# Kernel optimization log

Measured on AMD Instinct MI355X. Metric: run time of the kernel, lower is better.

Reference implementation:

```python
import jax, jax.numpy as jnp
import numpy as np

B, S, HID = 2, 2048, 2048
NH, NKV, D = 32, 8, 128
EPS = 1e-06
ROPE_BASE = 1000000.0


def _rope_tables(seq_len, dim, base):
    inv_freq = 1.0 / (base ** (jnp.arange(0, dim, 2, dtype=jnp.float32) / dim))
    t = jnp.arange(seq_len, dtype=jnp.float32)
    freqs = jnp.einsum('i,j->ij', t, inv_freq)          # [S, D/2]
    emb = jnp.concatenate([freqs, freqs], axis=-1)      # [S, D]
    return emb[None, None].astype(jnp.float32)          # [1,1,S,D] (pre cos/sin)


def setup_inputs() -> dict:
    key = jax.random.key(0)
    ks = jax.random.split(key, 6)
    emb = _rope_tables(S, D, ROPE_BASE)
    return {
        'hidden_states': jax.random.normal(ks[0], (B, S, HID), jnp.float32),
        'cos': jnp.cos(emb),
        'sin': jnp.sin(emb),
        'wq': jax.random.normal(ks[1], (NH * D, HID), jnp.float32) * 0.02,
        'wk': jax.random.normal(ks[2], (NKV * D, HID), jnp.float32) * 0.02,
        'wv': jax.random.normal(ks[3], (NKV * D, HID), jnp.float32) * 0.02,
        'wo': jax.random.normal(ks[4], (HID, NH * D), jnp.float32) * 0.02,
        'q_norm_w': jnp.ones((D,), jnp.float32),
        'k_norm_w': jnp.ones((D,), jnp.float32),
    }


def _rmsnorm(x, w, eps=EPS):
    xf = x.astype(jnp.float32)
    var = jnp.mean(xf * xf, axis=-1, keepdims=True)
    return (w * (xf * jax.lax.rsqrt(var + eps))).astype(x.dtype)


def _rotate_half(x):
    x1, x2 = jnp.split(x, 2, axis=-1)
    return jnp.concatenate([-x2, x1], axis=-1)


def reference(hidden_states, cos, sin, wq, wk, wv, wo, q_norm_w, k_norm_w):
    b, s, _ = hidden_states.shape
    groups = NH // NKV
    # projections -> [b, heads, s, d]
    q = (hidden_states @ wq.T).reshape(b, s, NH, D).transpose(0, 2, 1, 3)
    k = (hidden_states @ wk.T).reshape(b, s, NKV, D).transpose(0, 2, 1, 3)
    v = (hidden_states @ wv.T).reshape(b, s, NKV, D).transpose(0, 2, 1, 3)
    # per-head RMSNorm then RoPE
    q = _rmsnorm(q, q_norm_w)
    k = _rmsnorm(k, k_norm_w)
    q = q * cos + _rotate_half(q) * sin
    k = k * cos + _rotate_half(k) * sin
    # GQA expansion (repeat_interleave on head dim)
    k = jnp.repeat(k, groups, axis=1)
    v = jnp.repeat(v, groups, axis=1)
    # attention scores with additive causal bias of -10000 (as in source)
    scores = jnp.einsum('bhqd,bhkd->bhqk', q, k) / jnp.sqrt(jnp.float32(D))
    mask = jnp.triu(jnp.ones((s, s), jnp.float32), k=1)
    scores = scores - mask * 10000.0
    attn = jax.nn.softmax(scores.astype(jnp.float32), axis=-1).astype(q.dtype)
    out = jnp.einsum('bhqk,bhkd->bhqd', attn, v)
    out = out.transpose(0, 2, 1, 3).reshape(b, s, NH * D)
    return out @ wo.T
```

## Files before the change

### kernel.cpp

```cpp
#include <hip/hip_runtime.h>

typedef unsigned short u16;
typedef __attribute__((ext_vector_type(8))) short bf16x8;
typedef __attribute__((ext_vector_type(4))) float f32x4;
typedef __attribute__((ext_vector_type(2))) unsigned int u32x2;
typedef __attribute__((ext_vector_type(4))) unsigned int u32x4;

#define GAS __attribute__((address_space(1)))
#define LAS __attribute__((address_space(3)))
#define MFMA __builtin_amdgcn_mfma_f32_16x16x32_bf16
#define BAR() __builtin_amdgcn_s_barrier()
#define WAITV(n) asm volatile("s_waitcnt vmcnt(" #n ")" ::: "memory")

__device__ __forceinline__ void gload16(const void* g, void* l) {
  __builtin_amdgcn_global_load_lds((GAS void*)g, (LAS void*)l, 16, 0, 0);
}
__device__ __forceinline__ u16 f2b(float x) {
  union { float f; unsigned u; } c; c.f = x;
  unsigned r = c.u + 0x7fffu + ((c.u >> 16) & 1u);
  return (u16)(r >> 16);
}
__device__ __forceinline__ float b2f(u16 h) {
  union { unsigned u; float f; } c; c.u = ((unsigned)h) << 16;
  return c.f;
}
__device__ __forceinline__ unsigned cvtpk(float lo, float hi) {
  unsigned r;
  asm("v_cvt_pk_bf16_f32 %0, %1, %2" : "=v"(r) : "v"(lo), "v"(hi));
  return r;
}

__global__ __launch_bounds__(256) void cvt_all(
    const float* __restrict__ hs, const float* __restrict__ wq,
    const float* __restrict__ wk, const float* __restrict__ wv,
    const float* __restrict__ wo, u16* __restrict__ hsb,
    u16* __restrict__ wqkv, u16* __restrict__ wob) {
  int i = blockIdx.x * 256 + threadIdx.x;
  const float* src;
  u16* dst;
  int off;
  if (i < 1048576) {
    src = hs; dst = hsb; off = i;
  } else if (i < 2097152) {
    src = wq; dst = wqkv; off = i - 1048576;
  } else if (i < 2359296) {
    src = wk; dst = wqkv + 8388608; off = i - 2097152;
  } else if (i < 2621440) {
    src = wv; dst = wqkv + 10485760; off = i - 2359296;
  } else {
    src = wo; dst = wob; off = i - 2621440;
  }
  const float4* s4 = (const float4*)src;
  float4 a = s4[(size_t)off * 2], b = s4[(size_t)off * 2 + 1];
  u32x4 v;
  v[0] = (unsigned)f2b(a.x) | ((unsigned)f2b(a.y) << 16);
  v[1] = (unsigned)f2b(a.z) | ((unsigned)f2b(a.w) << 16);
  v[2] = (unsigned)f2b(b.x) | ((unsigned)f2b(b.y) << 16);
  v[3] = (unsigned)f2b(b.z) | ((unsigned)f2b(b.w) << 16);
  *(u32x4*)(dst + (size_t)off * 8) = v;
}

template <int MODE>
__global__ __launch_bounds__(512, 2) void gemm256(
    const u16* __restrict__ A, const u16* __restrict__ B,
    u16* __restrict__ Dq, u16* __restrict__ Dk, u16* __restrict__ Dv,
    float* __restrict__ Dout, float* __restrict__ Daux,
    const float* __restrict__ cosT, const float* __restrict__ sinT,
    const float* __restrict__ qnw, const float* __restrict__ knw,
    int Kstride, int KLEN, int tilesN, int nwg) {
  __shared__ __attribute__((aligned(16))) u16 lds[2][2][2][128 * 64];
  __shared__ float ssl[4][256];
  const int tid = threadIdx.x;
  const int lane = tid & 63;
  const int w = tid >> 6;
  const int wr = w >> 2, wc = w & 3;
  const int r = lane & 15, g = lane >> 4;

  int wg = blockIdx.x;
  const int cpx = nwg >> 3;
  wg = (wg & 7) * cpx + (wg >> 3);
  int sk = 0;
  if (MODE == 1) { sk = wg >> 7; wg &= 127; }
  const int bx = wg % tilesN, by = wg / tilesN;
  const size_t m0 = (size_t)by * 256, n0 = (size_t)bx * 256;
  const size_t koff = (size_t)sk * KLEN;
  const int NT = KLEN >> 6;

  auto stage = [&](int dbuf, int op, int half, int c, int k0) {
    int slot = c * 512 + tid;
    int row = slot >> 3;
    int kg = (slot & 7) ^ (row & 7);
    const u16* src = (op == 0)
        ? A + (m0 + half * 128 + row) * (size_t)Kstride + koff + k0 + kg * 8
        : B + (n0 + half * 128 + row) * (size_t)Kstride + koff + k0 + kg * 8;
    gload16(src, (char*)&lds[dbuf][op][half][0] + c * 8192 + w * 1024);
  };
  auto ldA = [&](int cur, int mi, int kk) -> bf16x8 {
    int rowl = mi * 16 + r;
    return *(const bf16x8*)((const char*)&lds[cur][0][wr][0] + rowl * 128 +
                            (((kk << 2) + g) ^ (rowl & 7)) * 16);
  };
  auto ldB = [&](int cur, int ni, int kk) -> bf16x8 {
    int rowl = (wc & 1) * 64 + ni * 16 + r;
    return *(const bf16x8*)((const char*)&lds[cur][1][wc >> 1][0] + rowl * 128 +
                            (((kk << 2) + g) ^ (rowl & 7)) * 16);
  };

  f32x4 acc[8][4];
#pragma unroll
  for (int i = 0; i < 8; ++i)
#pragma unroll
    for (int j = 0; j < 4; ++j) acc[i][j] = (f32x4){0.f, 0.f, 0.f, 0.f};

  stage(0, 1, 0, 0, 0); stage(0, 1, 0, 1, 0);
  stage(0, 1, 1, 0, 0); stage(0, 1, 1, 1, 0);
  stage(0, 0, 0, 0, 0); stage(0, 0, 1, 0, 0);
  stage(0, 0, 0, 1, 0); stage(0, 0, 1, 1, 0);
  WAITV(2);
  BAR();

  bf16x8 bf_[4][2];

#define GPHASE(MI0, IS0, IS1, WAITCODE)                                    \
  {                                                                        \
    bf16x8 aA0 = ldA(cur, MI0, 0), aA1 = ldA(cur, MI0, 1);                 \
    bf16x8 aB0 = ldA(cur, MI0 + 1, 0), aB1 = ldA(cur, MI0 + 1, 1);         \
    IS0; IS1;                                                              \
    BAR();                                                                 \
    __builtin_amdgcn_s_setprio(1);                                         \
    _Pragma("unroll") for (int ni = 0; ni < 4; ++ni) {                     \
      acc[MI0][ni] = MFMA(aA0, bf_[ni][0], acc[MI0][ni], 0, 0, 0);         \
      acc[MI0][ni] = MFMA(aA1, bf_[ni][1], acc[MI0][ni], 0, 0, 0);         \
      acc[MI0 + 1][ni] = MFMA(aB0, bf_[ni][0], acc[MI0 + 1][ni], 0, 0, 0); \
      acc[MI0 + 1][ni] = MFMA(aB1, bf_[ni][1], acc[MI0 + 1][ni], 0, 0, 0); \
    }                                                                      \
    __builtin_amdgcn_s_setprio(0);                                         \
    WAITCODE;                                                              \
    BAR();                                                                 \
  }

  for (int t = 0; t < NT - 1; ++t) {
    const int cur = t & 1, nb = cur ^ 1;
    const int k1 = (t + 1) << 6;
#pragma unroll
    for (int ni = 0; ni < 4; ++ni) {
      bf_[ni][0] = ldB(cur, ni, 0);
      bf_[ni][1] = ldB(cur, ni, 1);
    }
    GPHASE(0, stage(nb, 1, 0, 0, k1), stage(nb, 1, 0, 1, k1), );
    GPHASE(2, stage(nb, 1, 1, 0, k1), stage(nb, 1, 1, 1, k1), WAITV(4));
    GPHASE(4, stage(nb, 0, 0, 0, k1), stage(nb, 0, 1, 0, k1), );
    GPHASE(6, stage(nb, 0, 0, 1, k1), stage(nb, 0, 1, 1, k1), WAITV(2));
  }
  {
    const int cur = (NT - 1) & 1;
#pragma unroll
    for (int ni = 0; ni < 4; ++ni) {
      bf_[ni][0] = ldB(cur, ni, 0);
      bf_[ni][1] = ldB(cur, ni, 1);
    }
    GPHASE(0, , , );
    GPHASE(2, , , WAITV(0));
    GPHASE(4, , , );
    GPHASE(6, , , );
  }
#undef GPHASE

  if (MODE == 1) {
    float* pbase = (sk == 0) ? Dout : Daux;
#pragma unroll
    for (int mi = 0; mi < 8; ++mi)
#pragma unroll
      for (int ni = 0; ni < 4; ++ni)
#pragma unroll
        for (int j = 0; j < 4; ++j) {
          int m = (int)m0 + wr * 128 + mi * 16 + g * 4 + j;
          int n = (int)n0 + wc * 64 + ni * 16 + r;
          pbase[(size_t)m * (size_t)(tilesN * 256) + n] = acc[mi][ni][j];
        }
    return;
  }

  u16* lt = (u16*)&lds[0][0][0][0];

  if (bx < 20) {
    const bool isQ = (bx < 16);
    const float* nw = isQ ? qnw : knw;
    const float osc = isQ ? (0.08838834764831845f * 1.4426950408889634f) : 1.0f;

#pragma unroll
    for (int mi = 0; mi < 8; ++mi)
#pragma unroll
      for (int j = 0; j < 4; ++j) {
        float sq = 0.f;
#pragma unroll
        for (int ni = 0; ni < 4; ++ni) {
          float v = acc[mi][ni][j];
          sq += v * v;
        }
        sq += __shfl_xor(sq, 1);
        sq += __shfl_xor(sq, 2);
        sq += __shfl_xor(sq, 4);
        sq += __shfl_xor(sq, 8);
        ssl[wc][wr * 128 + mi * 16 + g * 4 + j] = sq;
      }
    BAR();

#pragma unroll
    for (int mi = 0; mi < 8; ++mi)
#pragma unroll
      for (int j = 0; j < 4; ++j) {
        int ml = wr * 128 + mi * 16 + g * 4 + j;
        float ss = ssl[wc & 2][ml] + ssl[(wc & 2) | 1][ml];
        float inv = rsqrtf(ss * (1.0f / 128.0f) + 1e-6f);
#pragma unroll
        for (int ni = 0; ni < 4; ++ni) {
          int d = (wc & 1) * 64 + ni * 16 + r;
          lt[ml * 256 + wc * 64 + ni * 16 + r] = f2b(acc[mi][ni][j] * inv * nw[d]);
        }
      }
    BAR();

#pragma unroll
    for (int t8 = 0; t8 < 8; ++t8) {
      int task = t8 * 512 + tid;
      int ml = task >> 4;
      int hd = (task >> 3) & 1;
      int gp = task & 7;
      int d0 = gp * 8;
      u32x4 xl = *(const u32x4*)(lt + ml * 256 + hd * 128 + d0);
      u32x4 xh = *(const u32x4*)(lt + ml * 256 + hd * 128 + 64 + d0);
      int m = (int)m0 + ml;
      int b = m >> 11, s = m & 2047;
      const float* cb = cosT + s * 128 + d0;
      const float* sb = sinT + s * 128 + d0;
      float4 c0a = *(const float4*)(cb), c0b = *(const float4*)(cb + 4);
      float4 s0a = *(const float4*)(sb), s0b = *(const float4*)(sb + 4);
      float4 c1a = *(const float4*)(cb + 64), c1b = *(const float4*)(cb + 68);
      float4 s1a = *(const float4*)(sb + 64), s1b = *(const float4*)(sb + 68);
      float x0[8], x1[8];
#pragma unroll
      for (int e = 0; e < 4; ++e) {
        x0[2 * e] = b2f((u16)(xl[e] & 0xffffu));
        x0[2 * e + 1] = b2f((u16)(xl[e] >> 16));
        x1[2 * e] = b2f((u16)(xh[e] & 0xffffu));
        x1[2 * e + 1] = b2f((u16)(xh[e] >> 16));
      }
      float c0[8] = {c0a.x, c0a.y, c0a.z, c0a.w, c0b.x, c0b.y, c0b.z, c0b.w};
      float s0[8] = {s0a.x, s0a.y, s0a.z, s0a.w, s0b.x, s0b.y, s0b.z, s0b.w};
      float c1[8] = {c1a.x, c1a.y, c1a.z, c1a.w, c1b.x, c1b.y, c1b.z, c1b.w};
      float s1[8] = {s1a.x, s1a.y, s1a.z, s1a.w, s1b.x, s1b.y, s1b.z, s1b.w};
      u32x4 y0, y1;
#pragma unroll
      for (int e = 0; e < 4; ++e) {
        float a0 = (x0[2 * e] * c0[2 * e] - x1[2 * e] * s0[2 * e]) * osc;
        float a1 = (x0[2 * e + 1] * c0[2 * e + 1] - x1[2 * e + 1] * s0[2 * e + 1]) * osc;
        y0[e] = cvtpk(a0, a1);
        float b0 = (x1[2 * e] * c1[2 * e] + x0[2 * e] * s1[2 * e]) * osc;
        float b1 = (x1[2 * e + 1] * c1[2 * e + 1] + x0[2 * e + 1] * s1[2 * e + 1]) * osc;
        y1[e] = cvtpk(b0, b1);
      }
      if (isQ) {
        int hq = 2 * bx + hd;
        u16* dst = Dq + (((size_t)b * 32 + hq) * 2048 + s) * 128 + d0;
        *(u32x4*)dst = y0;
        *(u32x4*)(dst + 64) = y1;
      } else {
        int hk = 2 * (bx - 16) + hd;
        u16* dst = Dk + (((size_t)b * 8 + hk) * 2048 + s) * 128 + d0;
        *(u32x4*)dst = y0;
        *(u32x4*)(dst + 64) = y1;
      }
    }
  } else {
#pragma unroll
    for (int mi = 0; mi < 8; ++mi)
#pragma unroll
      for (int ni = 0; ni < 4; ++ni)
#pragma unroll
        for (int j = 0; j < 4; ++j) {
          int ml = wr * 128 + mi * 16 + g * 4 + j;
          int nl = wc * 64 + ni * 16 + r;
          int gm = ml >> 3;
          lt[nl * 256 + (((gm ^ (nl & 7)) << 3) | (ml & 7))] = f2b(acc[mi][ni][j]);
        }
    BAR();
#pragma unroll
    for (int t16 = 0; t16 < 16; ++t16) {
      int task = t16 * 512 + tid;
      int nl = task >> 5;
      int mg = task & 31;
      u32x4 v = *(const u32x4*)(lt + nl * 256 + ((mg ^ (nl & 7)) << 3));
      int hv = 2 * (bx - 20) + (nl >> 7);
      int d = nl & 127;
      int m = (int)m0 + mg * 8;
      int b = m >> 11, s = m & 2047;
      *(u32x4*)(Dv + (((size_t)b * 8 + hv) * 128 + d) * 2048 + s) = v;
    }
  }
}

__global__ __launch_bounds__(256) void reduce_add(const float* __restrict__ P0,
                                                  const float* __restrict__ P1,
                                                  float* __restrict__ out, int n4) {
  int i = blockIdx.x * 256 + threadIdx.x;
  if (i >= n4) return;
  float4 a = ((const float4*)P0)[i];
  float4 b = ((const float4*)P1)[i];
  a.x += b.x; a.y += b.y; a.z += b.z; a.w += b.w;
  ((float4*)out)[i] = a;
}

__global__ __launch_bounds__(256, 2) void attn_fwd(const u16* __restrict__ Q,
                                                   const u16* __restrict__ Kg,
                                                   const u16* __restrict__ Vg,
                                                   u16* __restrict__ AO) {
  __shared__ __attribute__((aligned(16))) u16 Ks[2][64 * 128];
  __shared__ __attribute__((aligned(16))) u16 Vt[2][128 * 64];
  __shared__ __attribute__((aligned(16))) u16 Plds[4][32 * 64];
  const int tid = threadIdx.x;
  const int lane = tid & 63;
  const int w = tid >> 6;
  const int r = lane & 15, g = lane >> 4;
  const int p = blockIdx.x, h = blockIdx.y, b = blockIdx.z;
  const int hkv = h >> 2;

  const u16* Kp = Kg + (((size_t)b * 8 + hkv) * 2048) * 128;
  const u16* Vp = Vg + (((size_t)b * 8 + hkv) * 128) * 2048;

  const short one_bf = (short)0x3F80;
  const bf16x8 vones = {one_bf, one_bf, one_bf, one_bf, one_bf, one_bf, one_bf, one_bf};

#pragma unroll 1
  for (int phase = 0; phase < 2; ++phase) {
    const int qt = phase == 0 ? (15 - p) : p;
    const u16* Qp = Q + (((size_t)b * 32 + h) * 2048 + qt * 128 + w * 32) * 128;

    bf16x8 qf[2][4];
#pragma unroll
    for (int f = 0; f < 2; ++f)
#pragma unroll
      for (int kk = 0; kk < 4; ++kk)
        qf[f][kk] = *(const bf16x8*)(Qp + (f * 16 + r) * 128 + kk * 32 + g * 8);

    f32x4 off[2][8];
#pragma unroll
    for (int f = 0; f < 2; ++f)
#pragma unroll
      for (int i = 0; i < 8; ++i) off[f][i] = (f32x4){0.f, 0.f, 0.f, 0.f};
    f32x4 lr4[2] = {(f32x4){0.f, 0.f, 0.f, 0.f}, (f32x4){0.f, 0.f, 0.f, 0.f}};
    const int qg0 = qt * 128 + w * 32 + r;
    const int qg1 = qg0 + 16;

    const u16* kst[4];
    const u16* vst[4];
#pragma unroll
    for (int c = 0; c < 4; ++c) {
      int t = c * 256 + tid;
      kst[c] = Kp + (size_t)(t >> 4) * 128 + (size_t)(((t & 15) ^ ((t >> 4) & 7)) * 8);
      int d = t >> 3;
      vst[c] = Vp + (size_t)d * 2048 + (size_t)(((t & 7) ^ ((d >> 1) & 7)) * 8);
    }
    auto stageKV = [&](int buf) {
#pragma unroll
      for (int c = 0; c < 4; ++c) {
        gload16(kst[c], (char*)&Ks[buf][0] + c * 4096 + w * 1024);
        kst[c] += 64 * 128;
      }
#pragma unroll
      for (int c = 0; c < 4; ++c) {
        gload16(vst[c], (char*)&Vt[buf][0] + c * 4096 + w * 1024);
        vst[c] += 64;
      }
    };

    const int nu = 2 * qt + 2;

    stageKV(0);
    WAITV(0);
    BAR();

    for (int kt = 0; kt < nu; ++kt) {
      const int cur = kt & 1;
      if (kt + 1 < nu) stageKV(cur ^ 1);

      const char* KsC = (const char*)&Ks[cur][0];
      const char* VtC = (const char*)&Vt[cur][0];

      f32x4 sc0[4], sc1[4];
#pragma unroll
      for (int ni = 0; ni < 4; ++ni) {
        f32x4 a0 = (f32x4){0.f, 0.f, 0.f, 0.f};
        f32x4 a1 = (f32x4){0.f, 0.f, 0.f, 0.f};
        int ro = ni * 16 + r;
#pragma unroll
        for (int kk = 0; kk < 4; ++kk) {
          int slot = (ro * 16 + kk * 4 + g) ^ (ro & 7);
          bf16x8 kf = *(const bf16x8*)(KsC + slot * 16);
          a0 = MFMA(kf, qf[0][kk], a0, 0, 0, 0);
          a1 = MFMA(kf, qf[1][kk], a1, 0, 0, 0);
        }
        sc0[ni] = a0;
        sc1[ni] = a1;
      }

      if (kt >= 2 * qt) {
#pragma unroll
        for (int ni = 0; ni < 4; ++ni)
#pragma unroll
          for (int j = 0; j < 4; ++j) {
            int kvg = kt * 64 + ni * 16 + g * 4 + j;
            sc0[ni][j] = (kvg > qg0) ? -1e30f : sc0[ni][j];
            sc1[ni][j] = (kvg > qg1) ? -1e30f : sc1[ni][j];
          }
      }

      {
        char* pw = (char*)&Plds[w][0];
        int sw = (r & 7) << 4;
#pragma unroll
        for (int ni = 0; ni < 4; ++ni) {
          u32x2 pr0, pr1;
          pr0[0] = cvtpk(exp2f(sc0[ni][0]), exp2f(sc0[ni][1]));
          pr0[1] = cvtpk(exp2f(sc0[ni][2]), exp2f(sc0[ni][3]));
          pr1[0] = cvtpk(exp2f(sc1[ni][0]), exp2f(sc1[ni][1]));
          pr1[1] = cvtpk(exp2f(sc1[ni][2]), exp2f(sc1[ni][3]));
          *(u32x2*)(pw + ((r * 128 + ni * 32 + g * 8) ^ sw)) = pr0;
          *(u32x2*)(pw + (((16 + r) * 128 + ni * 32 + g * 8) ^ sw)) = pr1;
        }
      }
      bf16x8 pa[2][2];
      {
        const char* pw = (const char*)&Plds[w][0];
        int sw = (r & 7) << 4;
#pragma unroll
        for (int kk = 0; kk < 2; ++kk) {
          pa[0][kk] = *(const bf16x8*)(pw + ((r * 128 + kk * 64 + g * 16) ^ sw));
          pa[1][kk] = *(const bf16x8*)(pw + (((16 + r) * 128 + kk * 64 + g * 16) ^ sw));
        }
      }

      lr4[0] = MFMA(pa[0][0], vones, lr4[0], 0, 0, 0);
      lr4[0] = MFMA(pa[0][1], vones, lr4[0], 0, 0, 0);
      lr4[1] = MFMA(pa[1][0], vones, lr4[1], 0, 0, 0);
      lr4[1] = MFMA(pa[1][1], vones, lr4[1], 0, 0, 0);

#pragma unroll
      for (int dd = 0; dd < 8; ++dd) {
        int d = dd * 16 + r;
#pragma unroll
        for (int kk = 0; kk < 2; ++kk) {
          int ph = (kk * 4 + g) ^ ((r >> 1) & 7);
          bf16x8 vf = *(const bf16x8*)(VtC + (size_t)d * 128 + ph * 16);
          off[0][dd] = MFMA(pa[0][kk], vf, off[0][dd], 0, 0, 0);
          off[1][dd] = MFMA(pa[1][kk], vf, off[1][dd], 0, 0, 0);
        }
      }

      WAITV(0);
      BAR();
    }

#pragma unroll
    for (int f = 0; f < 2; ++f) {
      f32x4 il4;
#pragma unroll
      for (int j = 0; j < 4; ++j) il4[j] = 1.0f / lr4[f][j];
      const size_t ob = (size_t)b * 2048 + qt * 128 + w * 32 + f * 16 + g * 4;
#pragma unroll
      for (int dd = 0; dd < 8; ++dd) {
        AO[(ob + 0) * 4096 + h * 128 + dd * 16 + r] = f2b(off[f][dd][0] * il4[0]);
        AO[(ob + 1) * 4096 + h * 128 + dd * 16 + r] = f2b(off[f][dd][1] * il4[1]);
        AO[(ob + 2) * 4096 + h * 128 + dd * 16 + r] = f2b(off[f][dd][2] * il4[2]);
        AO[(ob + 3) * 4096 + h * 128 + dd * 16 + r] = f2b(off[f][dd][3] * il4[3]);
      }
    }
  }
}

extern "C" void kernel_launch(void* const* d_in, const int* in_sizes, int n_in,
                              void* d_out, int out_size, void* d_ws, size_t ws_size,
                              hipStream_t stream) {
  (void)in_sizes; (void)n_in; (void)out_size; (void)ws_size;
  const float* hs = (const float*)d_in[0];
  const float* cosT = (const float*)d_in[1];
  const float* sinT = (const float*)d_in[2];
  const float* wq = (const float*)d_in[3];
  const float* wk = (const float*)d_in[4];
  const float* wv = (const float*)d_in[5];
  const float* wo = (const float*)d_in[6];
  const float* qnw = (const float*)d_in[7];
  const float* knw = (const float*)d_in[8];
  float* out = (float*)d_out;

  char* ws = (char*)d_ws;
  u16* hsb  = (u16*)(ws);
  u16* wqkv = (u16*)(ws + 16777216);
  u16* wob  = (u16*)(ws + 41943040);
  u16* Qb   = (u16*)(ws + 58720256);
  u16* Kb   = (u16*)(ws + 92274688);
  u16* VTb  = (u16*)(ws + 100663296);
  u16* AO   = (u16*)(ws + 109051904);
  float* P0 = (float*)(ws + 58720256);
  float* P1 = (float*)(ws);

  cvt_all<<<14336, 256, 0, stream>>>(hs, wq, wk, wv, wo, hsb, wqkv, wob);

  gemm256<0><<<384, 512, 0, stream>>>(hsb, wqkv, Qb, Kb, VTb, nullptr, nullptr,
                                      cosT, sinT, qnw, knw, 2048, 2048, 24, 384);

  attn_fwd<<<dim3(8, 32, 2), 256, 0, stream>>>(Qb, Kb, VTb, AO);

  gemm256<1><<<256, 512, 0, stream>>>(AO, wob, nullptr, nullptr, nullptr, P0, P1,
                                      nullptr, nullptr, nullptr, nullptr,
                                      4096, 2048, 8, 256);
  reduce_add<<<8192, 256, 0, stream>>>(P0, P1, out, 2097152);
}
```

Before: 331.5 us.

## Move Q RMSNorm and RoPE from projection epilogue into attention Q load

```diff
diff --git a/kernel.cpp b/kernel.cpp
--- a/kernel.cpp
+++ b/kernel.cpp
@@ -66,7 +66,7 @@
     u16* __restrict__ Dq, u16* __restrict__ Dk, u16* __restrict__ Dv,
     float* __restrict__ Dout, float* __restrict__ Daux,
     const float* __restrict__ cosT, const float* __restrict__ sinT,
-    const float* __restrict__ qnw, const float* __restrict__ knw,
+    const float* __restrict__ knw,
     int Kstride, int KLEN, int tilesN, int nwg) {
   __shared__ __attribute__((aligned(16))) u16 lds[2][2][2][128 * 64];
   __shared__ float ssl[4][256];
@@ -183,11 +183,20 @@
 
   u16* lt = (u16*)&lds[0][0][0][0];
 
-  if (bx < 20) {
-    const bool isQ = (bx < 16);
-    const float* nw = isQ ? qnw : knw;
-    const float osc = isQ ? (0.08838834764831845f * 1.4426950408889634f) : 1.0f;
-
+  if (bx < 16) {
+#pragma unroll
+    for (int mi = 0; mi < 8; ++mi)
+#pragma unroll
+      for (int ni = 0; ni < 4; ++ni)
+#pragma unroll
+        for (int j = 0; j < 4; ++j) {
+          int m = (int)m0 + wr * 128 + mi * 16 + g * 4 + j;
+          int n = (int)n0 + wc * 64 + ni * 16 + r;
+          int b = m >> 11, s = m & 2047;
+          Dq[(((size_t)b * 32 + (n >> 7)) * 2048 + s) * 128 + (n & 127)] =
+              f2b(acc[mi][ni][j]);
+        }
+  } else if (bx < 20) {
 #pragma unroll
     for (int mi = 0; mi < 8; ++mi)
 #pragma unroll
@@ -205,7 +214,6 @@
         ssl[wc][wr * 128 + mi * 16 + g * 4 + j] = sq;
       }
     BAR();
-
 #pragma unroll
     for (int mi = 0; mi < 8; ++mi)
 #pragma unroll
@@ -216,11 +224,10 @@
 #pragma unroll
         for (int ni = 0; ni < 4; ++ni) {
           int d = (wc & 1) * 64 + ni * 16 + r;
-          lt[ml * 256 + wc * 64 + ni * 16 + r] = f2b(acc[mi][ni][j] * inv * nw[d]);
+          lt[ml * 256 + wc * 64 + ni * 16 + r] = f2b(acc[mi][ni][j] * inv * knw[d]);
         }
       }
     BAR();
-
 #pragma unroll
     for (int t8 = 0; t8 < 8; ++t8) {
       int task = t8 * 512 + tid;
@@ -234,10 +241,8 @@
       int b = m >> 11, s = m & 2047;
       const float* cb = cosT + s * 128 + d0;
       const float* sb = sinT + s * 128 + d0;
-      float4 c0a = *(const float4*)(cb), c0b = *(const float4*)(cb + 4);
-      float4 s0a = *(const float4*)(sb), s0b = *(const float4*)(sb + 4);
-      float4 c1a = *(const float4*)(cb + 64), c1b = *(const float4*)(cb + 68);
-      float4 s1a = *(const float4*)(sb + 64), s1b = *(const float4*)(sb + 68);
+      float4 ca = *(const float4*)(cb), cb4 = *(const float4*)(cb + 4);
+      float4 sa = *(const float4*)(sb), sb4 = *(const float4*)(sb + 4);
       float x0[8], x1[8];
 #pragma unroll
       for (int e = 0; e < 4; ++e) {
@@ -246,31 +251,22 @@
         x1[2 * e] = b2f((u16)(xh[e] & 0xffffu));
         x1[2 * e + 1] = b2f((u16)(xh[e] >> 16));
       }
-      float c0[8] = {c0a.x, c0a.y, c0a.z, c0a.w, c0b.x, c0b.y, c0b.z, c0b.w};
-      float s0[8] = {s0a.x, s0a.y, s0a.z, s0a.w, s0b.x, s0b.y, s0b.z, s0b.w};
-      float c1[8] = {c1a.x, c1a.y, c1a.z, c1a.w, c1b.x, c1b.y, c1b.z, c1b.w};
-      float s1[8] = {s1a.x, s1a.y, s1a.z, s1a.w, s1b.x, s1b.y, s1b.z, s1b.w};
+      float cc[8] = {ca.x, ca.y, ca.z, ca.w, cb4.x, cb4.y, cb4.z, cb4.w};
+      float sc[8] = {sa.x, sa.y, sa.z, sa.w, sb4.x, sb4.y, sb4.z, sb4.w};
       u32x4 y0, y1;
 #pragma unroll
       for (int e = 0; e < 4; ++e) {
-        float a0 = (x0[2 * e] * c0[2 * e] - x1[2 * e] * s0[2 * e]) * osc;
-        float a1 = (x0[2 * e + 1] * c0[2 * e + 1] - x1[2 * e + 1] * s0[2 * e + 1]) * osc;
+        float a0 = x0[2 * e] * cc[2 * e] - x1[2 * e] * sc[2 * e];
+        float a1 = x0[2 * e + 1] * cc[2 * e + 1] - x1[2 * e + 1] * sc[2 * e + 1];
         y0[e] = cvtpk(a0, a1);
-        float b0 = (x1[2 * e] * c1[2 * e] + x0[2 * e] * s1[2 * e]) * osc;
-        float b1 = (x1[2 * e + 1] * c1[2 * e + 1] + x0[2 * e + 1] * s1[2 * e + 1]) * osc;
+        float b0 = x1[2 * e] * cc[2 * e] + x0[2 * e] * sc[2 * e];
+        float b1 = x1[2 * e + 1] * cc[2 * e + 1] + x0[2 * e + 1] * sc[2 * e + 1];
         y1[e] = cvtpk(b0, b1);
       }
-      if (isQ) {
-        int hq = 2 * bx + hd;
-        u16* dst = Dq + (((size_t)b * 32 + hq) * 2048 + s) * 128 + d0;
-        *(u32x4*)dst = y0;
-        *(u32x4*)(dst + 64) = y1;
-      } else {
-        int hk = 2 * (bx - 16) + hd;
-        u16* dst = Dk + (((size_t)b * 8 + hk) * 2048 + s) * 128 + d0;
-        *(u32x4*)dst = y0;
-        *(u32x4*)(dst + 64) = y1;
-      }
+      int hk = 2 * (bx - 16) + hd;
+      u16* dst = Dk + (((size_t)b * 8 + hk) * 2048 + s) * 128 + d0;
+      *(u32x4*)dst = y0;
+      *(u32x4*)(dst + 64) = y1;
     }
   } else {
 #pragma unroll
@@ -311,10 +307,11 @@
   ((float4*)out)[i] = a;
 }
 
-__global__ __launch_bounds__(256, 2) void attn_fwd(const u16* __restrict__ Q,
-                                                   const u16* __restrict__ Kg,
-                                                   const u16* __restrict__ Vg,
-                                                   u16* __restrict__ AO) {
+__global__ __launch_bounds__(256, 2) void attn_fwd(
+    const u16* __restrict__ Q, const u16* __restrict__ Kg,
+    const u16* __restrict__ Vg, u16* __restrict__ AO,
+    const float* __restrict__ cosT, const float* __restrict__ sinT,
+    const float* __restrict__ qnw) {
   __shared__ __attribute__((aligned(16))) u16 Ks[2][64 * 128];
   __shared__ __attribute__((aligned(16))) u16 Vt[2][128 * 64];
   __shared__ __attribute__((aligned(16))) u16 Plds[4][32 * 64];
@@ -330,6 +327,16 @@
 
   const short one_bf = (short)0x3F80;
   const bf16x8 vones = {one_bf, one_bf, one_bf, one_bf, one_bf, one_bf, one_bf, one_bf};
+  const float osc_q = 0.08838834764831845f * 1.4426950408889634f;
+
+  float nwv[4][8];
+#pragma unroll
+  for (int kk = 0; kk < 4; ++kk) {
+    float4 na = *(const float4*)(qnw + kk * 32 + g * 8);
+    float4 nb = *(const float4*)(qnw + kk * 32 + g * 8 + 4);
+    nwv[kk][0] = na.x; nwv[kk][1] = na.y; nwv[kk][2] = na.z; nwv[kk][3] = na.w;
+    nwv[kk][4] = nb.x; nwv[kk][5] = nb.y; nwv[kk][6] = nb.z; nwv[kk][7] = nb.w;
+  }
 
 #pragma unroll 1
   for (int phase = 0; phase < 2; ++phase) {
@@ -338,10 +345,55 @@
 
     bf16x8 qf[2][4];
 #pragma unroll
-    for (int f = 0; f < 2; ++f)
-#pragma unroll
-      for (int kk = 0; kk < 4; ++kk)
-        qf[f][kk] = *(const bf16x8*)(Qp + (f * 16 + r) * 128 + kk * 32 + g * 8);
+    for (int f = 0; f < 2; ++f) {
+      float xw[4][8];
+      float ssq = 0.f;
+#pragma unroll
+      for (int kk = 0; kk < 4; ++kk) {
+        bf16x8 raw = *(const bf16x8*)(Qp + (f * 16 + r) * 128 + kk * 32 + g * 8);
+        u32x4 rw = __builtin_bit_cast(u32x4, raw);
+#pragma unroll
+        for (int e2 = 0; e2 < 4; ++e2) {
+          float lo = b2f((u16)(rw[e2] & 0xffffu));
+          float hi = b2f((u16)(rw[e2] >> 16));
+          ssq += lo * lo + hi * hi;
+          xw[kk][2 * e2] = lo * nwv[kk][2 * e2];
+          xw[kk][2 * e2 + 1] = hi * nwv[kk][2 * e2 + 1];
+        }
+      }
+      ssq += __shfl_xor(ssq, 16);
+      ssq += __shfl_xor(ssq, 32);
+      float invs = rsqrtf(ssq * (1.0f / 128.0f) + 1e-6f) * osc_q;
+
+      const int srow = qt * 128 + w * 32 + f * 16 + r;
+      float cv[2][8], sv[2][8];
+#pragma unroll
+      for (int kh = 0; kh < 2; ++kh) {
+        const float* cb = cosT + srow * 128 + kh * 32 + g * 8;
+        const float* sb = sinT + srow * 128 + kh * 32 + g * 8;
+        float4 c1 = *(const float4*)cb, c2 = *(const float4*)(cb + 4);
+        float4 s1 = *(const float4*)sb, s2 = *(const float4*)(sb + 4);
+        cv[kh][0] = c1.x; cv[kh][1] = c1.y; cv[kh][2] = c1.z; cv[kh][3] = c1.w;
+        cv[kh][4] = c2.x; cv[kh][5] = c2.y; cv[kh][6] = c2.z; cv[kh][7] = c2.w;
+        sv[kh][0] = s1.x; sv[kh][1] = s1.y; sv[kh][2] = s1.z; sv[kh][3] = s1.w;
+        sv[kh][4] = s2.x; sv[kh][5] = s2.y; sv[kh][6] = s2.z; sv[kh][7] = s2.w;
+      }
+#pragma unroll
+      for (int kk = 0; kk < 4; ++kk) {
+        const int kh = kk & 1;
+        const float sgn = (kk < 2) ? -1.0f : 1.0f;
+        u32x4 yw;
+#pragma unroll
+        for (int e2 = 0; e2 < 4; ++e2) {
+          float y0 = (xw[kk][2 * e2] * cv[kh][2 * e2] +
+                      sgn * xw[kk ^ 2][2 * e2] * sv[kh][2 * e2]) * invs;
+          float y1 = (xw[kk][2 * e2 + 1] * cv[kh][2 * e2 + 1] +
+                      sgn * xw[kk ^ 2][2 * e2 + 1] * sv[kh][2 * e2 + 1]) * invs;
+          yw[e2] = cvtpk(y0, y1);
+        }
+        qf[f][kk] = __builtin_bit_cast(bf16x8, yw);
+      }
+    }
 
     f32x4 off[2][8];
 #pragma unroll
@@ -507,12 +559,12 @@
   cvt_all<<<14336, 256, 0, stream>>>(hs, wq, wk, wv, wo, hsb, wqkv, wob);
 
   gemm256<0><<<384, 512, 0, stream>>>(hsb, wqkv, Qb, Kb, VTb, nullptr, nullptr,
-                                      cosT, sinT, qnw, knw, 2048, 2048, 24, 384);
-
-  attn_fwd<<<dim3(8, 32, 2), 256, 0, stream>>>(Qb, Kb, VTb, AO);
+                                      cosT, sinT, knw, 2048, 2048, 24, 384);
+
+  attn_fwd<<<dim3(8, 32, 2), 256, 0, stream>>>(Qb, Kb, VTb, AO, cosT, sinT, qnw);
 
   gemm256<1><<<256, 512, 0, stream>>>(AO, wob, nullptr, nullptr, nullptr, P0, P1,
-                                      nullptr, nullptr, nullptr, nullptr,
+                                      nullptr, nullptr, nullptr,
                                       4096, 2048, 8, 256);
   reduce_add<<<8192, 256, 0, stream>>>(P0, P1, out, 2097152);
 }
```

After: 334.6 us. Within noise of the previous version (+0.9%).
